# Kernel tuning notes

Hardware: AMD Instinct MI355X
Metric: run time of the kernel (lower is better)

The kernel has to match this reference:

```python
import jax, jax.numpy as jnp
import numpy as np
from math import factorial, comb

N_NODES = 50000
N_EDGES = 640000
FEAT = 32
NUM_BASIS = 8
CUTOFF = 5.0
MAX_Z = 118
NUM_ITERS = 3
LMAX = 2
K = (LMAX + 1) ** 2  # 9 spherical channels for max_degree=2


def _assoc_legendre(c, s, lmax):
    # associated Legendre P_l^m without Condon-Shortley phase
    P = {(0, 0): np.ones_like(c)}
    for m in range(1, lmax + 1):
        P[(m, m)] = P[(m - 1, m - 1)] * (2 * m - 1) * s
    for m in range(lmax):
        P[(m + 1, m)] = (2 * m + 1) * c * P[(m, m)]
    for m in range(lmax + 1):
        for l in range(m + 2, lmax + 1):
            P[(l, m)] = ((2 * l - 1) * c * P[(l - 1, m)] - (l + m - 1) * P[(l - 2, m)]) / (l - m)
    return P


def _real_sh_np(xyz, lmax):
    # Racah-normalized real spherical harmonics (Y_00 = 1), order m=-l..l
    r = np.linalg.norm(xyz, axis=1)
    cth = xyz[:, 2] / r
    sth = np.sqrt(np.maximum(1.0 - cth ** 2, 0.0))
    phi = np.arctan2(xyz[:, 1], xyz[:, 0])
    P = _assoc_legendre(cth, sth, lmax)
    cols = []
    for l in range(lmax + 1):
        for m in range(-l, l + 1):
            am = abs(m)
            if m == 0:
                cols.append(P[(l, 0)])
            else:
                nrm = np.sqrt(2.0 * factorial(l - am) / factorial(l + am))
                ang = np.cos(am * phi) if m > 0 else np.sin(am * phi)
                cols.append(nrm * P[(l, am)] * ang)
    return np.stack(cols, axis=1)


def _gaunt_tensor():
    # cg[k1,k2,k3]: expansion of Y_k1 * Y_k2 onto Y_k3 (degrees <= 2).
    # Products of degree<=2 harmonics lie exactly in span of degree<=4 harmonics,
    # so the least-squares fit below recovers exact coefficients.
    rng = np.random.default_rng(0)
    pts = rng.normal(size=(4096, 3))
    pts /= np.linalg.norm(pts, axis=1, keepdims=True)
    A = _real_sh_np(pts, 2 * LMAX)  # (M, 25)
    Y = A[:, :K]                    # (M, 9)
    prod = (Y[:, :, None] * Y[:, None, :]).reshape(len(pts), K * K)
    coef, *_ = np.linalg.lstsq(A, prod, rcond=None)  # (25, 81)
    return coef[:K].reshape(K, K, K).transpose(1, 2, 0).astype(np.float32)


CG = jnp.asarray(_gaunt_tensor())  # (9, 9, 9)
LOG_BINOM = jnp.asarray([np.log(comb(NUM_BASIS - 1, kk)) for kk in range(NUM_BASIS)], dtype=jnp.float32)


def _sh_l2(u):
    # Racah real SH of unit vectors, degrees 0..2, order m=-l..l
    x, y, z = u[:, 0], u[:, 1], u[:, 2]
    s3 = 1.7320508075688772
    return jnp.stack([
        jnp.ones_like(x),
        y, z, x,
        s3 * x * y, s3 * y * z, 0.5 * (3.0 * z * z - 1.0), s3 * x * z, 0.5 * s3 * (x * x - y * y),
    ], axis=1)


def _radial(r):
    # reciprocal Bernstein basis (log-space, stable) * smooth cutoff
    u = r / (1.0 + r)
    k = jnp.arange(NUM_BASIS, dtype=jnp.float32)
    n = float(NUM_BASIS - 1)
    eps = 1e-12
    logu = jnp.log(jnp.maximum(u, eps))[:, None]
    log1u = jnp.log(jnp.maximum(1.0 - u, eps))[:, None]
    bern = jnp.exp(LOG_BINOM + k * logu + (n - k) * log1u)  # (E, B)
    cut = jnp.where(r < CUTOFF, jnp.exp(-(r * r) / jnp.maximum(CUTOFF * CUTOFF - r * r, eps)), 0.0)
    return bern * cut[:, None]


def _forward(dr_vec, embed, rad_w, d1w, d1b, d2w, d2b, Z, neighbor_idxs):
    idx_i, idx_j = neighbor_idxs[0], neighbor_idxs[1]
    r = jnp.linalg.norm(dr_vec, axis=1)
    u = dr_vec / jnp.maximum(r, 1e-9)[:, None]
    Ysh = _sh_l2(u)              # (E, 9) angular basis
    rad = _radial(r)             # (E, B) radial basis
    # mask padding edges (idx_i == idx_j) as in mask_by_neighbor
    rad = rad * (idx_i != idx_j).astype(rad.dtype)[:, None]

    N = Z.shape[0]
    x = jnp.zeros((N, K, FEAT), jnp.float32).at[:, 0, :].set(embed[Z])

    for i in range(NUM_ITERS):
        last = i == NUM_ITERS - 1
        k3 = 1 if last else K    # last MessagePass has max_degree=0
        xe = x[idx_j]                                  # (E, 9, F) edge gather
        g = jnp.einsum('eb,dbf->edf', rad, rad_w[i])   # (E, 3, F) radial->feature per basis degree
        y = jnp.zeros((N_EDGES, k3, FEAT), jnp.float32)
        for l2 in range(LMAX + 1):
            sl = slice(l2 * l2, (l2 + 1) ** 2)
            c = jnp.einsum('abc,eb->eac', CG[:, sl, :k3], Ysh[:, sl])          # (E, 9, k3)
            y = y + jnp.einsum('eac,eaf->ecf', c, xe * g[:, l2][:, None, :])   # (E, k3, F)
        m = jax.ops.segment_sum(y, idx_i, num_segments=N)                      # scatter-sum
        if last:
            x = x[:, :1, :]      # change_max_degree_or_type(x, 0)
        h = x + m
        h = jnp.einsum('nkf,fg->nkg', h, d1w[i]).at[:, 0, :].add(d1b[i])
        gate = jax.nn.sigmoid(h[:, :1, :])
        h = h * gate             # silu on scalar channel, sigmoid-gated tensor channels
        h = jnp.einsum('nkf,fg->nkg', h, d2w[i]).at[:, 0, :].add(d2b[i])
        x = x + h
    return x[:, 0, :]            # (N, F)


def setup_inputs() -> dict:
    key = jax.random.key(0)
    ks = jax.random.split(key, 8)
    dr_vec = jax.random.normal(ks[0], (N_EDGES, 3), jnp.float32) * 2.0
    Z = jax.random.randint(ks[1], (N_NODES,), 0, MAX_Z + 1, jnp.int32)
    neighbor_idxs = jax.random.randint(ks[2], (2, N_EDGES), 0, N_NODES, jnp.int32)
    embed = jax.random.normal(ks[3], (MAX_Z + 1, FEAT), jnp.float32)
    rad_w = jax.random.normal(ks[4], (NUM_ITERS, LMAX + 1, NUM_BASIS, FEAT), jnp.float32) * 0.5
    d1w = jax.random.normal(ks[5], (NUM_ITERS, FEAT, FEAT), jnp.float32) * (1.0 / np.sqrt(FEAT))
    d1b = jnp.zeros((NUM_ITERS, FEAT), jnp.float32)
    d2w = jax.random.normal(ks[6], (NUM_ITERS, FEAT, FEAT), jnp.float32) * 0.02
    d2b = jnp.zeros((NUM_ITERS, FEAT), jnp.float32)
    return {"dr_vec": dr_vec, "embed": embed, "rad_w": rad_w, "d1w": d1w, "d1b": d1b,
            "d2w": d2w, "d2b": d2b, "Z": Z, "neighbor_idxs": neighbor_idxs}


def reference(dr_vec, embed, rad_w, d1w, d1b, d2w, d2b, Z, neighbor_idxs):
    return _forward(dr_vec, embed, rad_w, d1w, d1b, d2w, d2b, Z, neighbor_idxs)
```

## Files before the change

### kernel.cpp

```cpp
#include <hip/hip_runtime.h>
#include <hip/hip_fp16.h>
#include <math.h>

#define NN 50000
#define NE 640000
#define F  32
#define KCH 9
#define CUT 5.0f

#define C13 (1.0f/3.0f)
#define C23 (2.0f/3.0f)
#define C15 0.2f
#define C25 0.4f
#define C17 (1.0f/7.0f)
#define C27 (2.0f/7.0f)
#define IS3 0.5773502691896258f
#define S35 0.3464101615137755f
#define S37 0.2474358296526968f
#define S3  1.7320508075688772f

#define NBLK 2048
#define NHALF (NBLK * 8)

typedef _Float16 h2 __attribute__((ext_vector_type(2)));

union U2H { unsigned int u; __half2 h; };
union UH2 { unsigned int u; h2 v; };

__device__ __forceinline__ unsigned int pack2(float a, float b) {
    U2H c; c.h = __floats2half2_rn(a, b); return c.u;
}
__device__ __forceinline__ float2 unpack2(unsigned int u) {
    U2H c; c.u = u; return __half22float2(c.h);
}
__device__ __forceinline__ float h2f(ushort u) {
    return __half2float(__ushort_as_half(u));
}
__device__ __forceinline__ h2 as_h2(unsigned int u) { UH2 c; c.u = u; return c.v; }

__device__ __forceinline__ float fdot2f(h2 a, h2 b, float c) {
#if __has_builtin(__builtin_amdgcn_fdot2)
    return __builtin_amdgcn_fdot2(a, b, c, false);
#else
    return fmaf((float)a.x, (float)b.x, fmaf((float)a.y, (float)b.y, c));
#endif
}

__global__ __launch_bounds__(256) void init_x(const float* __restrict__ embed,
                                              const int* __restrict__ Z,
                                              float* __restrict__ x0,
                                              ushort* __restrict__ x0h,
                                              uint4* __restrict__ xhA,
                                              ushort* __restrict__ xhB) {
    int idx = blockIdx.x * 256 + threadIdx.x;
    int n = idx >> 5;
    float v = embed[Z[n] * F + (idx & 31)];
    x0[idx] = v;
    unsigned int p = pack2(v, 0.f);
    x0h[idx] = (ushort)(p & 0xFFFFu);
    uint4 ua; ua.x = p; ua.y = 0u; ua.z = 0u; ua.w = 0u;
    xhA[idx] = ua;
    xhB[idx] = 0;
}

__global__ __launch_bounds__(256) void hist_kernel(const int* __restrict__ idx_i,
                                                   const int* __restrict__ idx_j,
                                                   const float* __restrict__ dr,
                                                   int* __restrict__ cnt) {
    int e = blockIdx.x * 256 + threadIdx.x;
    if (e >= NE) return;
    int ni = idx_i[e], nj = idx_j[e];
    float dx = dr[3 * e + 0], dy = dr[3 * e + 1], dz = dr[3 * e + 2];
    float r2 = fmaf(dx, dx, fmaf(dy, dy, dz * dz));
    if (ni != nj && r2 < CUT * CUT) atomicAdd(&cnt[ni], 1);
}

#define SCAN_T 1024
#define SCAN_C ((NN + SCAN_T - 1) / SCAN_T)

__global__ __launch_bounds__(SCAN_T) void scan_kernel(const int* __restrict__ cnt,
                                                      int* __restrict__ offs,
                                                      int* __restrict__ head) {
    __shared__ int ps[SCAN_T];
    int t = threadIdx.x;
    int b = t * SCAN_C;
    int e = min(b + SCAN_C, NN);
    int s = 0;
    for (int i = b; i < e; ++i) s += cnt[i];
    ps[t] = s;
    __syncthreads();
    for (int off = 1; off < SCAN_T; off <<= 1) {
        int v = (t >= off) ? ps[t - off] : 0;
        __syncthreads();
        ps[t] += v;
        __syncthreads();
    }
    int run = (t == 0) ? 0 : ps[t - 1];
    for (int i = b; i < e; ++i) { int c = cnt[i]; offs[i] = run; head[i] = run; run += c; }
    if (t == SCAN_T - 1) offs[NN] = ps[SCAN_T - 1];
}

__global__ void pad_zero(const int* __restrict__ neptr,
                         uint4* __restrict__ geoA,
                         uint2* __restrict__ geoB,
                         ushort* __restrict__ njA) {
    int NEl = neptr[0];
    int i = threadIdx.x;
    if (i < 8) {
        uint4 z4; z4.x = z4.y = z4.z = z4.w = 0u;
        uint2 z2; z2.x = z2.y = 0u;
        geoA[NEl + i] = z4;
        geoB[NEl + i] = z2;
        njA[NEl + i] = 0;
    }
}

__global__ __launch_bounds__(256) void fill_kernel(const int* __restrict__ idx_i,
                                                   const int* __restrict__ idx_j,
                                                   const float* __restrict__ dr,
                                                   int* __restrict__ head,
                                                   uint4* __restrict__ geoA,
                                                   uint2* __restrict__ geoB,
                                                   ushort* __restrict__ njA) {
    int e = blockIdx.x * 256 + threadIdx.x;
    if (e >= NE) return;
    int ni = idx_i[e], nj = idx_j[e];
    float dx = dr[3 * e + 0], dy = dr[3 * e + 1], dz = dr[3 * e + 2];
    float r2 = fmaf(dx, dx, fmaf(dy, dy, dz * dz));
    if (!(ni != nj && r2 < CUT * CUT)) return;

    float r = sqrtf(r2);
    float inv = 1.0f / fmaxf(r, 1e-9f);
    float ux = dx * inv, uy = dy * inv, uz = dz * inv;

    float cut = expf(-r2 / fmaxf(CUT * CUT - r2, 1e-12f));
    float ur = r / (1.0f + r), vr = 1.0f - ur;
    float up2 = ur*ur, up3 = up2*ur, up4 = up3*ur, up5 = up4*ur, up6 = up5*ur, up7 = up6*ur;
    float vp2 = vr*vr, vp3 = vp2*vr, vp4 = vp3*vr, vp5 = vp4*vr, vp6 = vp5*vr, vp7 = vp6*vr;

    int p = atomicAdd(&head[ni], 1);
    uint4 gA;
    gA.x = pack2(ux, uy);
    gA.y = (pack2(uz, 0.f) & 0xFFFFu) | ((unsigned int)ni << 16);
    gA.z = pack2(cut * vp7,              cut * 7.f  * ur  * vp6);
    gA.w = pack2(cut * 21.f * up2 * vp5, cut * 35.f * up3 * vp4);
    uint2 gB;
    gB.x = pack2(cut * 35.f * up4 * vp3, cut * 21.f * up5 * vp2);
    gB.y = pack2(cut * 7.f  * up6 * vr,  cut * up7);
    geoA[p] = gA;
    geoB[p] = gB;
    njA[p] = (ushort)nj;
}

template<int MODE>
__device__ __forceinline__ void flush_acc(float* __restrict__ m, int cur, int f,
                                          float* __restrict__ acc) {
    if (cur < 0) return;
    if (MODE == 2) {
        unsafeAtomicAdd(m + (size_t)cur * F + f, acc[0]);
    } else {
        float* mp = m + (size_t)cur * KCH * F + f;
        #pragma unroll
        for (int a = 0; a < KCH; ++a) unsafeAtomicAdd(mp + a * F, acc[a]);
    }
}

template<int MODE>
__device__ __forceinline__ void edge_compute(uint4 gA, uint2 gB, uint4 xav, ushort x8v,
                                             const h2* __restrict__ rwh,
                                             float* __restrict__ acc, int& cur,
                                             float* __restrict__ m, int f) {
    constexpr int NACC = (MODE == 2) ? 1 : KCH;
    int dst = (int)(gA.y >> 16);
    if (dst != cur) {
        flush_acc<MODE>(m, cur, f, acc);
        cur = dst;
        #pragma unroll
        for (int a = 0; a < NACC; ++a) acc[a] = 0.f;
    }

    float2 uxy = unpack2(gA.x);
    float ux = uxy.x, uy = uxy.y;
    float uz = h2f((ushort)(gA.y & 0xFFFFu));
    h2 rc01 = as_h2(gA.z), rc23 = as_h2(gA.w), rc45 = as_h2(gB.x), rc67 = as_h2(gB.y);

    float g0 = fdot2f(rc67, rwh[3],  fdot2f(rc45, rwh[2],  fdot2f(rc23, rwh[1],  fdot2f(rc01, rwh[0], 0.f))));
    float g1 = fdot2f(rc67, rwh[7],  fdot2f(rc45, rwh[6],  fdot2f(rc23, rwh[5],  fdot2f(rc01, rwh[4], 0.f))));
    float g2 = fdot2f(rc67, rwh[11], fdot2f(rc45, rwh[10], fdot2f(rc23, rwh[9],  fdot2f(rc01, rwh[8], 0.f))));

    if (MODE == 0) {
        float xe0 = h2f(x8v);
        float s2 = S3 * g2;
        acc[0] = fmaf(xe0, g0, acc[0]);
        acc[1] = fmaf(xe0, uy * g1, acc[1]);
        acc[2] = fmaf(xe0, uz * g1, acc[2]);
        acc[3] = fmaf(xe0, ux * g1, acc[3]);
        acc[4] = fmaf(xe0, s2 * ux * uy, acc[4]);
        acc[5] = fmaf(xe0, s2 * uy * uz, acc[5]);
        acc[6] = fmaf(xe0, fmaf(1.5f * uz, uz, -0.5f) * g2, acc[6]);
        acc[7] = fmaf(xe0, s2 * ux * uz, acc[7]);
        acc[8] = fmaf(xe0, 0.5f * s2 * (ux * ux - uy * uy), acc[8]);
    } else {
        float xe[9];
        {
            float2 p;
            p = unpack2(xav.x); xe[0] = p.x; xe[1] = p.y;
            p = unpack2(xav.y); xe[2] = p.x; xe[3] = p.y;
            p = unpack2(xav.z); xe[4] = p.x; xe[5] = p.y;
            p = unpack2(xav.w); xe[6] = p.x; xe[7] = p.y;
            xe[8] = h2f(x8v);
        }
        if (MODE == 2) {
            float dot1 = uy * xe[1];
            dot1 = fmaf(uz, xe[2], dot1);
            dot1 = fmaf(ux, xe[3], dot1);
            float Y4 = S3 * ux * uy, Y5 = S3 * uy * uz, Y7 = S3 * ux * uz;
            float Y6 = fmaf(1.5f * uz, uz, -0.5f);
            float Y8 = 0.5f * S3 * (ux * ux - uy * uy);
            float dot2 = Y4 * xe[4];
            dot2 = fmaf(Y5, xe[5], dot2);
            dot2 = fmaf(Y6, xe[6], dot2);
            dot2 = fmaf(Y7, xe[7], dot2);
            dot2 = fmaf(Y8, xe[8], dot2);
            acc[0] = fmaf(g0, xe[0], acc[0]);
            acc[0] = fmaf(g1, dot1, acc[0]);
            acc[0] = fmaf(g2, dot2, acc[0]);
        } else {
            float s2 = S3 * g2;
            float w[9];
            w[0] = g0;
            w[1] = uy * g1; w[2] = uz * g1; w[3] = ux * g1;
            w[4] = s2 * ux * uy;
            w[5] = s2 * uy * uz;
            w[6] = fmaf(1.5f * uz, uz, -0.5f) * g2;
            w[7] = s2 * ux * uz;
            w[8] = 0.5f * s2 * (ux * ux - uy * uy);

            float d0v = xe[0]*w[0], d1v = xe[1]*w[1], d2v = xe[2]*w[2], d3v = xe[3]*w[3];
            float d4v = xe[4]*w[4], d5v = xe[5]*w[5], d6v = xe[6]*w[6], d7v = xe[7]*w[7];
            float d8v = xe[8]*w[8];

            acc[0] += d0v + C13 * (d1v + d2v + d3v) + C15 * (d4v + d5v + d6v + d7v + d8v);
            #define T(a, b) (xe[a] * w[b] + xe[b] * w[a])
            acc[1] += T(0,1) - C15 * T(1,6) - S35 * T(1,8) + S35 * T(2,5) + S35 * T(3,4);
            acc[2] += T(0,2) + S35 * T(1,5) + C25 * T(2,6) + S35 * T(3,7);
            acc[3] += T(0,3) + S35 * T(1,4) + S35 * T(2,7) - C15 * T(3,6) + S35 * T(3,8);
            acc[4] += T(0,4) + IS3 * T(1,3) - C27 * T(4,6) + S37 * T(5,7);
            acc[5] += T(0,5) + IS3 * T(1,2) + S37 * T(4,7) + C17 * T(5,6) - S37 * T(5,8);
            acc[6] += T(0,6) - C13 * d1v + C23 * d2v - C13 * d3v
                    - C27 * d4v + C17 * d5v + C27 * d6v + C17 * d7v - C27 * d8v;
            acc[7] += T(0,7) + IS3 * T(2,3) + S37 * T(4,5) + C17 * T(6,7) + S37 * T(7,8);
            acc[8] += T(0,8) - IS3 * d1v + IS3 * d3v - S37 * d5v + S37 * d7v - C27 * T(6,8);
            #undef T
        }
    }
}

template<int MODE>
__global__ __launch_bounds__(256) void gather_kernel(const uint4* __restrict__ geoA,
                                                     const uint2* __restrict__ geoB,
                                                     const ushort* __restrict__ njA,
                                                     const ushort* __restrict__ x0h,
                                                     const uint4* __restrict__ xhA,
                                                     const ushort* __restrict__ xhB,
                                                     const float* __restrict__ rw_iter,
                                                     const int* __restrict__ neptr,
                                                     float* __restrict__ m) {
    int lane = threadIdx.x & 63;
    int wid  = threadIdx.x >> 6;
    int half = lane >> 5;
    int f    = lane & 31;
    int lb   = (blockIdx.x & 7) * (NBLK / 8) + (blockIdx.x >> 3);
    int h    = lb * 8 + wid * 2 + half;

    float rwf[24];
    #pragma unroll
    for (int lbq = 0; lbq < 24; ++lbq) rwf[lbq] = rw_iter[lbq * F + f];
    if (MODE == 2) {
        #pragma unroll
        for (int lbq = 8; lbq < 16; ++lbq) rwf[lbq] *= C13;
        #pragma unroll
        for (int lbq = 16; lbq < 24; ++lbq) rwf[lbq] *= C15;
    }
    h2 rwh[12];
    #pragma unroll
    for (int q = 0; q < 12; ++q) {
        h2 v; v.x = (_Float16)rwf[2 * q]; v.y = (_Float16)rwf[2 * q + 1];
        rwh[q] = v;
    }

    int NEl = neptr[0];
    int per = (NEl + NHALF - 1) / NHALF;
    int s = h * per;
    int e = min(s + per, NEl);
    if (s >= e) return;

    constexpr int NACC = (MODE == 2) ? 1 : KCH;
    float acc[NACC];
    #pragma unroll
    for (int a = 0; a < NACC; ++a) acc[a] = 0.f;
    int cur = -1;

    uint4 ga[4]; uint2 gb[4]; int njr[4];
    uint4 xa[2] = {}; ushort x80[2];
    #pragma unroll
    for (int p = 0; p < 4; ++p) {
        ga[p] = geoA[s + p];
        gb[p] = geoB[s + p];
        njr[p] = (int)njA[s + p + 2];
    }
    {
        int nj0 = (int)njA[s], nj1 = (int)njA[s + 1];
        if (MODE == 0) {
            x80[0] = x0h[nj0 * F + f];
            x80[1] = x0h[nj1 * F + f];
        } else {
            xa[0] = xhA[nj0 * F + f]; x80[0] = xhB[nj0 * F + f];
            xa[1] = xhA[nj1 * F + f]; x80[1] = xhB[nj1 * F + f];
        }
    }

    int t = s;
    while (t + 4 <= e) {
        #pragma unroll
        for (int p = 0; p < 4; ++p) {
            int x = t + p;
            uint4 gAv = ga[p]; uint2 gBv = gb[p];
            ga[p] = geoA[x + 4];
            gb[p] = geoB[x + 4];
            uint4 xav = xa[p & 1];
            ushort x8v = x80[p & 1];
            int njv = njr[p];
            if (MODE == 0) {
                x80[p & 1] = x0h[njv * F + f];
            } else {
                xa[p & 1] = xhA[njv * F + f];
                x80[p & 1] = xhB[njv * F + f];
            }
            njr[p] = (int)njA[x + 6];
            edge_compute<MODE>(gAv, gBv, xav, x8v, rwh, acc, cur, m, f);
        }
        t += 4;
    }
    for (; t < e; ++t) {
        uint4 gAv = geoA[t]; uint2 gBv = geoB[t];
        int njv = (int)njA[t];
        uint4 xav = {}; ushort x8v;
        if (MODE == 0) {
            x8v = x0h[njv * F + f];
        } else {
            xav = xhA[njv * F + f];
            x8v = xhB[njv * F + f];
        }
        edge_compute<MODE>(gAv, gBv, xav, x8v, rwh, acc, cur, m, f);
    }
    flush_acc<MODE>(m, cur, f, acc);
}

__global__ __launch_bounds__(256) void node_full(float* __restrict__ x0,
                                                 const float* __restrict__ m,
                                                 uint4* __restrict__ xhA,
                                                 ushort* __restrict__ xhB,
                                                 const float* __restrict__ w1,
                                                 const float* __restrict__ b1,
                                                 const float* __restrict__ w2,
                                                 const float* __restrict__ b2) {
    __shared__ float tile[8][KCH][F];
    int nl = threadIdx.x >> 5, f = threadIdx.x & 31;
    int n = blockIdx.x * 8 + nl;

    float w1c[F];
    #pragma unroll
    for (int fi = 0; fi < F; ++fi) w1c[fi] = w1[fi * F + f];

    float xk[KCH];
    {
        uint4 ua = xhA[n * F + f];
        ushort ub = xhB[n * F + f];
        float2 p;
        p = unpack2(ua.x); xk[0] = p.x; xk[1] = p.y;
        p = unpack2(ua.y); xk[2] = p.x; xk[3] = p.y;
        p = unpack2(ua.z); xk[4] = p.x; xk[5] = p.y;
        p = unpack2(ua.w); xk[6] = p.x; xk[7] = p.y;
        xk[8] = h2f(ub);
    }
    xk[0] = x0[n * F + f];

    #pragma unroll
    for (int k = 0; k < KCH; ++k)
        tile[nl][k][f] = xk[k] + m[((size_t)n * KCH + k) * F + f];
    __syncthreads();

    float o1[KCH];
    #pragma unroll
    for (int k = 0; k < KCH; ++k) {
        float s = 0.f;
        #pragma unroll
        for (int fi = 0; fi < F; ++fi) s = fmaf(tile[nl][k][fi], w1c[fi], s);
        o1[k] = s;
    }
    o1[0] += b1[f];
    float gate = 1.0f / (1.0f + expf(-o1[0]));
    __syncthreads();
    #pragma unroll
    for (int k = 0; k < KCH; ++k) tile[nl][k][f] = o1[k] * gate;
    __syncthreads();

    float w2c[F];
    #pragma unroll
    for (int fi = 0; fi < F; ++fi) w2c[fi] = w2[fi * F + f];

    float xn[KCH];
    #pragma unroll
    for (int k = 0; k < KCH; ++k) {
        float s = (k == 0) ? b2[f] : 0.f;
        #pragma unroll
        for (int fi = 0; fi < F; ++fi) s = fmaf(tile[nl][k][fi], w2c[fi], s);
        xn[k] = xk[k] + s;
    }

    x0[n * F + f] = xn[0];
    uint4 ua;
    ua.x = pack2(xn[0], xn[1]); ua.y = pack2(xn[2], xn[3]);
    ua.z = pack2(xn[4], xn[5]); ua.w = pack2(xn[6], xn[7]);
    xhA[n * F + f] = ua;
    xhB[n * F + f] = __half_as_ushort(__float2half_rn(xn[8]));
}

__global__ __launch_bounds__(256) void node_last(const float* __restrict__ x0,
                                                 const float* __restrict__ m1,
                                                 const float* __restrict__ w1,
                                                 const float* __restrict__ b1,
                                                 const float* __restrict__ w2,
                                                 const float* __restrict__ b2,
                                                 float* __restrict__ out) {
    __shared__ float tile[8][F];
    int nl = threadIdx.x >> 5, f = threadIdx.x & 31;
    int n = blockIdx.x * 8 + nl;

    float w1c[F];
    #pragma unroll
    for (int fi = 0; fi < F; ++fi) w1c[fi] = w1[fi * F + f];

    float xv = x0[n * F + f];
    tile[nl][f] = xv + m1[(size_t)n * F + f];
    __syncthreads();
    float s = 0.f;
    #pragma unroll
    for (int fi = 0; fi < F; ++fi) s = fmaf(tile[nl][fi], w1c[fi], s);
    s += b1[f];
    float gate = 1.0f / (1.0f + expf(-s));
    float h2v = s * gate;
    __syncthreads();
    tile[nl][f] = h2v;
    __syncthreads();
    float w2c[F];
    #pragma unroll
    for (int fi = 0; fi < F; ++fi) w2c[fi] = w2[fi * F + f];
    float o = b2[f];
    #pragma unroll
    for (int fi = 0; fi < F; ++fi) o = fmaf(tile[nl][fi], w2c[fi], o);
    out[(size_t)n * F + f] = xv + o;
}

extern "C" void kernel_launch(void* const* d_in, const int* in_sizes, int n_in,
                              void* d_out, int out_size, void* d_ws, size_t ws_size,
                              hipStream_t stream) {
    (void)in_sizes; (void)n_in; (void)out_size; (void)ws_size;
    const float* dr    = (const float*)d_in[0];
    const float* embed = (const float*)d_in[1];
    const float* rad_w = (const float*)d_in[2];
    const float* d1w   = (const float*)d_in[3];
    const float* d1b   = (const float*)d_in[4];
    const float* d2w   = (const float*)d_in[5];
    const float* d2b   = (const float*)d_in[6];
    const int*   Z     = (const int*)d_in[7];
    const int*   nidx  = (const int*)d_in[8];
    const int* idx_i = nidx;
    const int* idx_j = nidx + NE;

    uint4* xhA  = (uint4*)d_ws;
    float* m    = (float*)(xhA + (size_t)NN * F);
    float* x0   = m + (size_t)NN * KCH * F;
    ushort* x0h = (ushort*)(x0 + (size_t)NN * F);
    ushort* xhB = x0h + (size_t)NN * F;
    uint4* geoA = (uint4*)(xhB + (size_t)NN * F);
    uint2* geoB = (uint2*)(geoA + (size_t)NE + 8);
    ushort* njA = (ushort*)(geoB + (size_t)NE + 8);
    int* offs = (int*)(njA + (size_t)NE + 8);
    int* head = offs + (NN + 1);
    int* cnt  = head + NN;
    float* outp = (float*)d_out;

    size_t MB_full = (size_t)NN * KCH * F * sizeof(float);
    size_t MB_last = (size_t)NN * F * sizeof(float);

    hipMemsetAsync(cnt, 0, NN * sizeof(int), stream);
    hist_kernel<<<(NE + 255) / 256, 256, 0, stream>>>(idx_i, idx_j, dr, cnt);
    scan_kernel<<<1, SCAN_T, 0, stream>>>(cnt, offs, head);
    pad_zero<<<1, 64, 0, stream>>>(offs + NN, geoA, geoB, njA);
    fill_kernel<<<(NE + 255) / 256, 256, 0, stream>>>(idx_i, idx_j, dr, head, geoA, geoB, njA);

    init_x<<<NN * F / 256, 256, 0, stream>>>(embed, Z, x0, x0h, xhA, xhB);

    const int* neptr = offs + NN;
    for (int i = 0; i < 3; ++i) {
        const float* rwi = rad_w + (size_t)i * 3 * 8 * F;
        const float* w1 = d1w + (size_t)i * F * F;
        const float* b1 = d1b + (size_t)i * F;
        const float* w2 = d2w + (size_t)i * F * F;
        const float* b2 = d2b + (size_t)i * F;
        if (i == 0) {
            hipMemsetAsync(m, 0, MB_full, stream);
            gather_kernel<0><<<NBLK, 256, 0, stream>>>(geoA, geoB, njA, x0h, xhA, xhB, rwi, neptr, m);
            node_full<<<NN / 8, 256, 0, stream>>>(x0, m, xhA, xhB, w1, b1, w2, b2);
        } else if (i == 1) {
            hipMemsetAsync(m, 0, MB_full, stream);
            gather_kernel<1><<<NBLK, 256, 0, stream>>>(geoA, geoB, njA, x0h, xhA, xhB, rwi, neptr, m);
            node_full<<<NN / 8, 256, 0, stream>>>(x0, m, xhA, xhB, w1, b1, w2, b2);
        } else {
            hipMemsetAsync(m, 0, MB_last, stream);
            gather_kernel<2><<<NBLK, 256, 0, stream>>>(geoA, geoB, njA, x0h, xhA, xhB, rwi, neptr, m);
            node_last<<<NN / 8, 256, 0, stream>>>(x0, m, w1, b1, w2, b2, outp);
        }
    }
}
```

Before: 571.9 us.

## Simplify gather loop prefetch and replace fp16 dot2 radial with fp32 FMAs

Removes the 4-deep unrolled software pipeline of geometry loads. It is replaced by a simple per-edge loop that prefetches only the next neighbor's features one edge ahead and the neighbor index three ahead. The radial weights are now kept in fp32 and applied with scalar FMAs instead of packed fp16 dot2 instructions. The goals are lower register pressure and no tail loop, but geometry loads are now issued in the same iteration that uses them, so latency hiding is shallower and the radial step needs more ALU instructions.

After: 591.0 us. 1.03x slower.

```diff
diff --git a/kernel.cpp b/kernel.cpp
--- a/kernel.cpp
+++ b/kernel.cpp
@@ -22,10 +22,7 @@
 #define NBLK 2048
 #define NHALF (NBLK * 8)
 
-typedef _Float16 h2 __attribute__((ext_vector_type(2)));
-
 union U2H { unsigned int u; __half2 h; };
-union UH2 { unsigned int u; h2 v; };
 
 __device__ __forceinline__ unsigned int pack2(float a, float b) {
     U2H c; c.h = __floats2half2_rn(a, b); return c.u;
@@ -35,15 +32,6 @@
 }
 __device__ __forceinline__ float h2f(ushort u) {
     return __half2float(__ushort_as_half(u));
-}
-__device__ __forceinline__ h2 as_h2(unsigned int u) { UH2 c; c.u = u; return c.v; }
-
-__device__ __forceinline__ float fdot2f(h2 a, h2 b, float c) {
-#if __has_builtin(__builtin_amdgcn_fdot2)
-    return __builtin_amdgcn_fdot2(a, b, c, false);
-#else
-    return fmaf((float)a.x, (float)b.x, fmaf((float)a.y, (float)b.y, c));
-#endif
 }
 
 __global__ __launch_bounds__(256) void init_x(const float* __restrict__ embed,
@@ -162,97 +150,6 @@
         float* mp = m + (size_t)cur * KCH * F + f;
         #pragma unroll
         for (int a = 0; a < KCH; ++a) unsafeAtomicAdd(mp + a * F, acc[a]);
-    }
-}
-
-template<int MODE>
-__device__ __forceinline__ void edge_compute(uint4 gA, uint2 gB, uint4 xav, ushort x8v,
-                                             const h2* __restrict__ rwh,
-                                             float* __restrict__ acc, int& cur,
-                                             float* __restrict__ m, int f) {
-    constexpr int NACC = (MODE == 2) ? 1 : KCH;
-    int dst = (int)(gA.y >> 16);
-    if (dst != cur) {
-        flush_acc<MODE>(m, cur, f, acc);
-        cur = dst;
-        #pragma unroll
-        for (int a = 0; a < NACC; ++a) acc[a] = 0.f;
-    }
-
-    float2 uxy = unpack2(gA.x);
-    float ux = uxy.x, uy = uxy.y;
-    float uz = h2f((ushort)(gA.y & 0xFFFFu));
-    h2 rc01 = as_h2(gA.z), rc23 = as_h2(gA.w), rc45 = as_h2(gB.x), rc67 = as_h2(gB.y);
-
-    float g0 = fdot2f(rc67, rwh[3],  fdot2f(rc45, rwh[2],  fdot2f(rc23, rwh[1],  fdot2f(rc01, rwh[0], 0.f))));
-    float g1 = fdot2f(rc67, rwh[7],  fdot2f(rc45, rwh[6],  fdot2f(rc23, rwh[5],  fdot2f(rc01, rwh[4], 0.f))));
-    float g2 = fdot2f(rc67, rwh[11], fdot2f(rc45, rwh[10], fdot2f(rc23, rwh[9],  fdot2f(rc01, rwh[8], 0.f))));
-
-    if (MODE == 0) {
-        float xe0 = h2f(x8v);
-        float s2 = S3 * g2;
-        acc[0] = fmaf(xe0, g0, acc[0]);
-        acc[1] = fmaf(xe0, uy * g1, acc[1]);
-        acc[2] = fmaf(xe0, uz * g1, acc[2]);
-        acc[3] = fmaf(xe0, ux * g1, acc[3]);
-        acc[4] = fmaf(xe0, s2 * ux * uy, acc[4]);
-        acc[5] = fmaf(xe0, s2 * uy * uz, acc[5]);
-        acc[6] = fmaf(xe0, fmaf(1.5f * uz, uz, -0.5f) * g2, acc[6]);
-        acc[7] = fmaf(xe0, s2 * ux * uz, acc[7]);
-        acc[8] = fmaf(xe0, 0.5f * s2 * (ux * ux - uy * uy), acc[8]);
-    } else {
-        float xe[9];
-        {
-            float2 p;
-            p = unpack2(xav.x); xe[0] = p.x; xe[1] = p.y;
-            p = unpack2(xav.y); xe[2] = p.x; xe[3] = p.y;
-            p = unpack2(xav.z); xe[4] = p.x; xe[5] = p.y;
-            p = unpack2(xav.w); xe[6] = p.x; xe[7] = p.y;
-            xe[8] = h2f(x8v);
-        }
-        if (MODE == 2) {
-            float dot1 = uy * xe[1];
-            dot1 = fmaf(uz, xe[2], dot1);
-            dot1 = fmaf(ux, xe[3], dot1);
-            float Y4 = S3 * ux * uy, Y5 = S3 * uy * uz, Y7 = S3 * ux * uz;
-            float Y6 = fmaf(1.5f * uz, uz, -0.5f);
-            float Y8 = 0.5f * S3 * (ux * ux - uy * uy);
-            float dot2 = Y4 * xe[4];
-            dot2 = fmaf(Y5, xe[5], dot2);
-            dot2 = fmaf(Y6, xe[6], dot2);
-            dot2 = fmaf(Y7, xe[7], dot2);
-            dot2 = fmaf(Y8, xe[8], dot2);
-            acc[0] = fmaf(g0, xe[0], acc[0]);
-            acc[0] = fmaf(g1, dot1, acc[0]);
-            acc[0] = fmaf(g2, dot2, acc[0]);
-        } else {
-            float s2 = S3 * g2;
-            float w[9];
-            w[0] = g0;
-            w[1] = uy * g1; w[2] = uz * g1; w[3] = ux * g1;
-            w[4] = s2 * ux * uy;
-            w[5] = s2 * uy * uz;
-            w[6] = fmaf(1.5f * uz, uz, -0.5f) * g2;
-            w[7] = s2 * ux * uz;
-            w[8] = 0.5f * s2 * (ux * ux - uy * uy);
-
-            float d0v = xe[0]*w[0], d1v = xe[1]*w[1], d2v = xe[2]*w[2], d3v = xe[3]*w[3];
-            float d4v = xe[4]*w[4], d5v = xe[5]*w[5], d6v = xe[6]*w[6], d7v = xe[7]*w[7];
-            float d8v = xe[8]*w[8];
-
-            acc[0] += d0v + C13 * (d1v + d2v + d3v) + C15 * (d4v + d5v + d6v + d7v + d8v);
-            #define T(a, b) (xe[a] * w[b] + xe[b] * w[a])
-            acc[1] += T(0,1) - C15 * T(1,6) - S35 * T(1,8) + S35 * T(2,5) + S35 * T(3,4);
-            acc[2] += T(0,2) + S35 * T(1,5) + C25 * T(2,6) + S35 * T(3,7);
-            acc[3] += T(0,3) + S35 * T(1,4) + S35 * T(2,7) - C15 * T(3,6) + S35 * T(3,8);
-            acc[4] += T(0,4) + IS3 * T(1,3) - C27 * T(4,6) + S37 * T(5,7);
-            acc[5] += T(0,5) + IS3 * T(1,2) + S37 * T(4,7) + C17 * T(5,6) - S37 * T(5,8);
-            acc[6] += T(0,6) - C13 * d1v + C23 * d2v - C13 * d3v
-                    - C27 * d4v + C17 * d5v + C27 * d6v + C17 * d7v - C27 * d8v;
-            acc[7] += T(0,7) + IS3 * T(2,3) + S37 * T(4,5) + C17 * T(6,7) + S37 * T(7,8);
-            acc[8] += T(0,8) - IS3 * d1v + IS3 * d3v - S37 * d5v + S37 * d7v - C27 * T(6,8);
-            #undef T
-        }
     }
 }
 
@@ -273,20 +170,14 @@
     int lb   = (blockIdx.x & 7) * (NBLK / 8) + (blockIdx.x >> 3);
     int h    = lb * 8 + wid * 2 + half;
 
-    float rwf[24];
-    #pragma unroll
-    for (int lbq = 0; lbq < 24; ++lbq) rwf[lbq] = rw_iter[lbq * F + f];
+    float rwv[24];
+    #pragma unroll
+    for (int q = 0; q < 24; ++q) rwv[q] = rw_iter[q * F + f];
     if (MODE == 2) {
         #pragma unroll
-        for (int lbq = 8; lbq < 16; ++lbq) rwf[lbq] *= C13;
+        for (int q = 8; q < 16; ++q) rwv[q] *= C13;
         #pragma unroll
-        for (int lbq = 16; lbq < 24; ++lbq) rwf[lbq] *= C15;
-    }
-    h2 rwh[12];
-    #pragma unroll
-    for (int q = 0; q < 12; ++q) {
-        h2 v; v.x = (_Float16)rwf[2 * q]; v.y = (_Float16)rwf[2 * q + 1];
-        rwh[q] = v;
+        for (int q = 16; q < 24; ++q) rwv[q] *= C15;
     }
 
     int NEl = neptr[0];
@@ -301,58 +192,133 @@
     for (int a = 0; a < NACC; ++a) acc[a] = 0.f;
     int cur = -1;
 
-    uint4 ga[4]; uint2 gb[4]; int njr[4];
-    uint4 xa[2] = {}; ushort x80[2];
-    #pragma unroll
-    for (int p = 0; p < 4; ++p) {
-        ga[p] = geoA[s + p];
-        gb[p] = geoB[s + p];
-        njr[p] = (int)njA[s + p + 2];
-    }
+    int nj1 = (int)njA[s + 1];
+    int nj2 = (int)njA[s + 2];
+    uint4 xa_c = {};
+    ushort x8_c;
     {
-        int nj0 = (int)njA[s], nj1 = (int)njA[s + 1];
+        int nj_c = (int)njA[s];
         if (MODE == 0) {
-            x80[0] = x0h[nj0 * F + f];
-            x80[1] = x0h[nj1 * F + f];
+            x8_c = x0h[nj_c * F + f];
         } else {
-            xa[0] = xhA[nj0 * F + f]; x80[0] = xhB[nj0 * F + f];
-            xa[1] = xhA[nj1 * F + f]; x80[1] = xhB[nj1 * F + f];
+            xa_c = xhA[nj_c * F + f];
+            x8_c = xhB[nj_c * F + f];
         }
     }
 
-    int t = s;
-    while (t + 4 <= e) {
-        #pragma unroll
-        for (int p = 0; p < 4; ++p) {
-            int x = t + p;
-            uint4 gAv = ga[p]; uint2 gBv = gb[p];
-            ga[p] = geoA[x + 4];
-            gb[p] = geoB[x + 4];
-            uint4 xav = xa[p & 1];
-            ushort x8v = x80[p & 1];
-            int njv = njr[p];
-            if (MODE == 0) {
-                x80[p & 1] = x0h[njv * F + f];
+    for (int t = s; t < e; ++t) {
+        uint4 gA = geoA[t];
+        uint2 gB = geoB[t];
+
+        uint4 xa_n = {};
+        ushort x8_n;
+        if (MODE == 0) {
+            x8_n = x0h[nj1 * F + f];
+        } else {
+            xa_n = xhA[nj1 * F + f];
+            x8_n = xhB[nj1 * F + f];
+        }
+        int njt = (int)njA[t + 3];
+
+        int dst = (int)(gA.y >> 16);
+        if (dst != cur) {
+            flush_acc<MODE>(m, cur, f, acc);
+            cur = dst;
+            #pragma unroll
+            for (int a = 0; a < NACC; ++a) acc[a] = 0.f;
+        }
+
+        float2 uxy = unpack2(gA.x);
+        float ux = uxy.x, uy = uxy.y;
+        float uz = h2f((ushort)(gA.y & 0xFFFFu));
+        float2 rcA = unpack2(gA.z);
+        float2 rcB = unpack2(gA.w);
+        float2 rcC = unpack2(gB.x);
+        float2 rcD = unpack2(gB.y);
+
+        float g0, g1, g2;
+        g0 = rcA.x * rwv[0];
+        g0 = fmaf(rcA.y, rwv[1], g0); g0 = fmaf(rcB.x, rwv[2], g0); g0 = fmaf(rcB.y, rwv[3], g0);
+        g0 = fmaf(rcC.x, rwv[4], g0); g0 = fmaf(rcC.y, rwv[5], g0); g0 = fmaf(rcD.x, rwv[6], g0);
+        g0 = fmaf(rcD.y, rwv[7], g0);
+        g1 = rcA.x * rwv[8];
+        g1 = fmaf(rcA.y, rwv[9],  g1); g1 = fmaf(rcB.x, rwv[10], g1); g1 = fmaf(rcB.y, rwv[11], g1);
+        g1 = fmaf(rcC.x, rwv[12], g1); g1 = fmaf(rcC.y, rwv[13], g1); g1 = fmaf(rcD.x, rwv[14], g1);
+        g1 = fmaf(rcD.y, rwv[15], g1);
+        g2 = rcA.x * rwv[16];
+        g2 = fmaf(rcA.y, rwv[17], g2); g2 = fmaf(rcB.x, rwv[18], g2); g2 = fmaf(rcB.y, rwv[19], g2);
+        g2 = fmaf(rcC.x, rwv[20], g2); g2 = fmaf(rcC.y, rwv[21], g2); g2 = fmaf(rcD.x, rwv[22], g2);
+        g2 = fmaf(rcD.y, rwv[23], g2);
+
+        if (MODE == 0) {
+            float xe0 = h2f(x8_c);
+            float s2 = S3 * g2;
+            acc[0] = fmaf(xe0, g0, acc[0]);
+            acc[1] = fmaf(xe0, uy * g1, acc[1]);
+            acc[2] = fmaf(xe0, uz * g1, acc[2]);
+            acc[3] = fmaf(xe0, ux * g1, acc[3]);
+            acc[4] = fmaf(xe0, s2 * ux * uy, acc[4]);
+            acc[5] = fmaf(xe0, s2 * uy * uz, acc[5]);
+            acc[6] = fmaf(xe0, fmaf(1.5f * uz, uz, -0.5f) * g2, acc[6]);
+            acc[7] = fmaf(xe0, s2 * ux * uz, acc[7]);
+            acc[8] = fmaf(xe0, 0.5f * s2 * (ux * ux - uy * uy), acc[8]);
+        } else {
+            float xe[9];
+            {
+                float2 p;
+                p = unpack2(xa_c.x); xe[0] = p.x; xe[1] = p.y;
+                p = unpack2(xa_c.y); xe[2] = p.x; xe[3] = p.y;
+                p = unpack2(xa_c.z); xe[4] = p.x; xe[5] = p.y;
+                p = unpack2(xa_c.w); xe[6] = p.x; xe[7] = p.y;
+                xe[8] = h2f(x8_c);
+            }
+            if (MODE == 2) {
+                float dot1 = uy * xe[1];
+                dot1 = fmaf(uz, xe[2], dot1);
+                dot1 = fmaf(ux, xe[3], dot1);
+                float Y4 = S3 * ux * uy, Y5 = S3 * uy * uz, Y7 = S3 * ux * uz;
+                float Y6 = fmaf(1.5f * uz, uz, -0.5f);
+                float Y8 = 0.5f * S3 * (ux * ux - uy * uy);
+                float dot2 = Y4 * xe[4];
+                dot2 = fmaf(Y5, xe[5], dot2);
+                dot2 = fmaf(Y6, xe[6], dot2);
+                dot2 = fmaf(Y7, xe[7], dot2);
+                dot2 = fmaf(Y8, xe[8], dot2);
+                acc[0] = fmaf(g0, xe[0], acc[0]);
+                acc[0] = fmaf(g1, dot1, acc[0]);
+                acc[0] = fmaf(g2, dot2, acc[0]);
             } else {
-                xa[p & 1] = xhA[njv * F + f];
-                x80[p & 1] = xhB[njv * F + f];
+                float s2 = S3 * g2;
+                float w[9];
+                w[0] = g0;
+                w[1] = uy * g1; w[2] = uz * g1; w[3] = ux * g1;
+                w[4] = s2 * ux * uy;
+                w[5] = s2 * uy * uz;
+                w[6] = fmaf(1.5f * uz, uz, -0.5f) * g2;
+                w[7] = s2 * ux * uz;
+                w[8] = 0.5f * s2 * (ux * ux - uy * uy);
+
+                float d0v = xe[0]*w[0], d1v = xe[1]*w[1], d2v = xe[2]*w[2], d3v = xe[3]*w[3];
+                float d4v = xe[4]*w[4], d5v = xe[5]*w[5], d6v = xe[6]*w[6], d7v = xe[7]*w[7];
+                float d8v = xe[8]*w[8];
+
+                acc[0] += d0v + C13 * (d1v + d2v + d3v) + C15 * (d4v + d5v + d6v + d7v + d8v);
+                #define T(a, b) (xe[a] * w[b] + xe[b] * w[a])
+                acc[1] += T(0,1) - C15 * T(1,6) - S35 * T(1,8) + S35 * T(2,5) + S35 * T(3,4);
+                acc[2] += T(0,2) + S35 * T(1,5) + C25 * T(2,6) + S35 * T(3,7);
+                acc[3] += T(0,3) + S35 * T(1,4) + S35 * T(2,7) - C15 * T(3,6) + S35 * T(3,8);
+                acc[4] += T(0,4) + IS3 * T(1,3) - C27 * T(4,6) + S37 * T(5,7);
+                acc[5] += T(0,5) + IS3 * T(1,2) + S37 * T(4,7) + C17 * T(5,6) - S37 * T(5,8);
+                acc[6] += T(0,6) - C13 * d1v + C23 * d2v - C13 * d3v
+                        - C27 * d4v + C17 * d5v + C27 * d6v + C17 * d7v - C27 * d8v;
+                acc[7] += T(0,7) + IS3 * T(2,3) + S37 * T(4,5) + C17 * T(6,7) + S37 * T(7,8);
+                acc[8] += T(0,8) - IS3 * d1v + IS3 * d3v - S37 * d5v + S37 * d7v - C27 * T(6,8);
+                #undef T
             }
-            njr[p] = (int)njA[x + 6];
-            edge_compute<MODE>(gAv, gBv, xav, x8v, rwh, acc, cur, m, f);
         }
-        t += 4;
-    }
-    for (; t < e; ++t) {
-        uint4 gAv = geoA[t]; uint2 gBv = geoB[t];
-        int njv = (int)njA[t];
-        uint4 xav = {}; ushort x8v;
-        if (MODE == 0) {
-            x8v = x0h[njv * F + f];
-        } else {
-            xav = xhA[njv * F + f];
-            x8v = xhB[njv * F + f];
-        }
-        edge_compute<MODE>(gAv, gBv, xav, x8v, rwh, acc, cur, m, f);
+
+        xa_c = xa_n; x8_c = x8_n;
+        nj1 = nj2; nj2 = njt;
     }
     flush_acc<MODE>(m, cur, f, acc);
 }
```
